# Kernel optimization log

Measured on AMD Instinct MI355X. Metric: run time of the kernel, lower is better.

## Reference

```python
import jax, jax.numpy as jnp
import numpy as np

BASE_RES = 0.2
RES_FACTOR = (1.0 - BASE_RES) * 0.9
N_ATOMS = 1024
LATENT = 128
WINDOW = 512
HOP = WINDOW // 2
RES_SAMPLES = 32768
N_FRAMES = RES_SAMPLES // HOP  # 128


def setup_inputs() -> dict:
    key = jax.random.key(0)
    ks = jax.random.split(key, 6)
    x = jax.random.normal(ks[0], (16, 64, LATENT), dtype=jnp.float32)
    W_sel = jax.random.normal(ks[1], (N_ATOMS, LATENT), dtype=jnp.float32) * 0.1
    b_sel = jnp.zeros((N_ATOMS,), dtype=jnp.float32)
    W_mom = jax.random.normal(ks[2], (N_FRAMES, LATENT), dtype=jnp.float32) * 0.1
    b_mom = jnp.zeros((N_FRAMES,), dtype=jnp.float32)
    atoms = jax.random.normal(ks[3], (N_ATOMS, RES_SAMPLES), dtype=jnp.float32) * 0.01
    return {"x": x, "W_sel": W_sel, "b_sel": b_sel, "W_mom": W_mom, "b_mom": b_mom, "atoms": atoms}


def _hann_periodic(n):
    # torch.hann_window default (periodic=True)
    return 0.5 * (1.0 - jnp.cos(2.0 * jnp.pi * jnp.arange(n) / n))


def reference(x, W_sel, b_sel, W_mom, b_mom, atoms):
    # momentum: sigmoid -> affine -> log-cumsum-exp decay per frame
    mom = BASE_RES + jax.nn.sigmoid(jnp.einsum('bel,fl->bef', x, W_mom) + b_mom) * RES_FACTOR
    mom = jnp.exp(jnp.cumsum(jnp.log(1e-12 + mom), axis=-1))  # (B,E,F)

    # softmax atom selection and mixing
    sel = jax.nn.softmax(jnp.einsum('bel,al->bea', x, W_sel) + b_sel, axis=-1)
    res = jnp.einsum('bea,as->bes', sel, atoms)  # (B,E,S)

    # windowed_audio: pad by hop, unfold, apply hann window
    padded = jnp.pad(res, ((0, 0), (0, 0), (0, HOP)))
    idx = jnp.arange(N_FRAMES)[:, None] * HOP + jnp.arange(WINDOW)[None, :]
    frames = padded[..., idx] * _hann_periodic(WINDOW)  # (B,E,F,W)

    # per-frame unit norm, then momentum scaling
    norm = jnp.linalg.norm(frames, axis=-1, keepdims=True)
    frames = frames / (norm + 1e-8)
    frames = frames * mom[..., None]

    # overlap-add with hop = WINDOW//2 (no extra window)
    B, E = frames.shape[0], frames.shape[1]
    first = frames[..., :HOP].reshape(B, E, -1)
    second = frames[..., HOP:].reshape(B, E, -1)
    out = jnp.pad(first, ((0, 0), (0, 0), (0, HOP))) + jnp.pad(second, ((0, 0), (0, 0), (HOP, 0)))
    return out[..., :RES_SAMPLES], mom
```

## Files before the change

kernel.cpp:

```cpp
#include <hip/hip_runtime.h>


typedef __attribute__((ext_vector_type(8))) short short8;
typedef __attribute__((ext_vector_type(4))) float f32x4;

typedef __attribute__((address_space(1))) void GV;
typedef __attribute__((address_space(3))) void LV;

__device__ __forceinline__ unsigned short f2bf(float f) {
    union { float f; unsigned u; } c; c.f = f;
    unsigned u = c.u;
    u = (u + 0x7FFFu + ((u >> 16) & 1u)) >> 16;
    return (unsigned short)u;
}
__device__ __forceinline__ float bf2f(unsigned short h) {
    union { unsigned u; float f; } c; c.u = ((unsigned)h) << 16; return c.f;
}

__global__ __launch_bounds__(256) void k_convert(
        const float* __restrict__ x, const float* __restrict__ Wsel,
        unsigned short* __restrict__ xbf, unsigned short* __restrict__ wbf) {
    const int i = (blockIdx.x * 256 + threadIdx.x) * 4;
    {
        float4 v = *(const float4*)(x + i);
        uint2 q;
        q.x = (unsigned)f2bf(v.x) | ((unsigned)f2bf(v.y) << 16);
        q.y = (unsigned)f2bf(v.z) | ((unsigned)f2bf(v.w) << 16);
        *(uint2*)(xbf + i) = q;
    }
    {
        float4 v = *(const float4*)(Wsel + i);
        uint2 q;
        q.x = (unsigned)f2bf(v.x) | ((unsigned)f2bf(v.y) << 16);
        q.y = (unsigned)f2bf(v.z) | ((unsigned)f2bf(v.w) << 16);
        *(uint2*)(wbf + i) = q;
    }
}

__global__ __launch_bounds__(256) void k_head_gemm(
        const unsigned short* __restrict__ A, const unsigned short* __restrict__ Bm,
        float* __restrict__ logits) {
    __shared__ __align__(16) unsigned short lA[128 * 32];
    __shared__ __align__(16) unsigned short lB[128 * 32];
    const int tid = threadIdx.x;
    const int wave = tid >> 6;
    const int lane = tid & 63;
    const int l15 = lane & 15, quad = lane >> 4;
    const int i0 = blockIdx.x * 128;
    const int j0 = blockIdx.y * 128;
    const int wi = wave >> 1, wj = wave & 1;
    const int rsel = lane >> 2;
    const int koff = (lane & 3) * 8;

    f32x4 acc[4][4] = {};

    for (int kt = 0; kt < 4; ++kt) {
        const int kbase = kt * 32;
#pragma unroll
        for (int c = 0; c < 2; ++c) {
            const int row = c * 64 + wave * 16 + rsel;
            const unsigned short* ga = A + (size_t)(i0 + row) * 128 + kbase + koff;
            const unsigned short* gb = Bm + (size_t)(j0 + row) * 128 + kbase + koff;
            unsigned short* la = lA + (c * 64 + wave * 16) * 32;
            unsigned short* lb = lB + (c * 64 + wave * 16) * 32;
            __builtin_amdgcn_global_load_lds((GV*)ga, (LV*)la, 16, 0, 0);
            __builtin_amdgcn_global_load_lds((GV*)gb, (LV*)lb, 16, 0, 0);
        }
        __syncthreads();

        short8 af[4], bf[4];
#pragma unroll
        for (int ti = 0; ti < 4; ++ti)
            af[ti] = *(const short8*)(lA + (wi * 64 + ti * 16 + l15) * 32 + quad * 8);
#pragma unroll
        for (int tj = 0; tj < 4; ++tj)
            bf[tj] = *(const short8*)(lB + (wj * 64 + tj * 16 + l15) * 32 + quad * 8);
#pragma unroll
        for (int ti = 0; ti < 4; ++ti)
#pragma unroll
            for (int tj = 0; tj < 4; ++tj)
                acc[ti][tj] = __builtin_amdgcn_mfma_f32_16x16x32_bf16(
                    af[ti], bf[tj], acc[ti][tj], 0, 0, 0);
        __syncthreads();
    }

#pragma unroll
    for (int ti = 0; ti < 4; ++ti) {
#pragma unroll
        for (int tj = 0; tj < 4; ++tj) {
            const int mrow = j0 + wj * 64 + tj * 16 + l15;
            const int abase = i0 + wi * 64 + ti * 16 + quad * 4;
            f32x4 v = acc[ti][tj];
            float4 o; o.x = v[0]; o.y = v[1]; o.z = v[2]; o.w = v[3];
            *(float4*)(logits + (size_t)mrow * 1024 + abase) = o;
        }
    }
}

__global__ __launch_bounds__(256) void k_softmax_mom(
        const float* __restrict__ logits_g, const float* __restrict__ bsel,
        const float* __restrict__ x, const float* __restrict__ Wmom,
        const float* __restrict__ bmom, unsigned short* __restrict__ sel,
        float* __restrict__ momout) {
    __shared__ float xs[128];
    __shared__ float logits[1024];
    __shared__ float mvals[128];
    __shared__ float wred[4];
    __shared__ float sstat[2];
    const int tid = threadIdx.x;
    const int m = blockIdx.x;

    if (tid < 32) *(float4*)&xs[tid * 4] = *(const float4*)(x + (size_t)m * 128 + tid * 4);
    for (int a = tid; a < 1024; a += 256)
        logits[a] = logits_g[(size_t)m * 1024 + a] + bsel[a];
    __syncthreads();

    if (tid < 128) {
        const float4* w = (const float4*)(Wmom + (size_t)tid * 128);
        float acc = 0.f;
#pragma unroll
        for (int k = 0; k < 32; ++k) {
            float4 wv = w[k]; float4 xv = *(const float4*)&xs[k * 4];
            acc += wv.x * xv.x + wv.y * xv.y + wv.z * xv.z + wv.w * xv.w;
        }
        acc += bmom[tid];
        float sig = 1.f / (1.f + __expf(-acc));
        mvals[tid] = 0.2f + sig * 0.72f;
    }
    __syncthreads();

    float mx = -1e30f;
    for (int a = tid; a < 1024; a += 256) mx = fmaxf(mx, logits[a]);
#pragma unroll
    for (int off = 32; off; off >>= 1) mx = fmaxf(mx, __shfl_xor(mx, off, 64));
    if ((tid & 63) == 0) wred[tid >> 6] = mx;
    __syncthreads();
    if (tid == 0) sstat[0] = fmaxf(fmaxf(wred[0], wred[1]), fmaxf(wred[2], wred[3]));
    __syncthreads();
    mx = sstat[0];

    float psum = 0.f;
    for (int a = tid; a < 1024; a += 256) {
        float e = __expf(logits[a] - mx);
        logits[a] = e;
        psum += e;
    }
#pragma unroll
    for (int off = 32; off; off >>= 1) psum += __shfl_xor(psum, off, 64);
    if ((tid & 63) == 0) wred[tid >> 6] = psum;
    __syncthreads();
    if (tid == 0) sstat[1] = wred[0] + wred[1] + wred[2] + wred[3];
    __syncthreads();
    const float inv = 1.f / sstat[1];
    for (int a = tid; a < 1024; a += 256)
        sel[(size_t)m * 1024 + a] = f2bf(logits[a] * inv);

    if (tid == 0) {
        float p = 1.f;
        for (int f = 0; f < 128; ++f) {
            p *= (mvals[f] + 1e-12f);
            momout[(size_t)m * 128 + f] = p;
        }
    }
}

__global__ __launch_bounds__(256) void k_transpose(
        const float* __restrict__ atoms, unsigned short* __restrict__ atomsT) {
    __shared__ float t[64][65];
    const int tid = threadIdx.x;
    const int s0 = blockIdx.x * 64;
    const int a0 = blockIdx.y * 64;

    {
        const int r0 = tid >> 4;
        const int c4 = (tid & 15) * 4;
        for (int rr = r0; rr < 64; rr += 16) {
            float4 v = *(const float4*)(atoms + (size_t)(a0 + rr) * 32768 + s0 + c4);
            t[rr][c4] = v.x; t[rr][c4 + 1] = v.y; t[rr][c4 + 2] = v.z; t[rr][c4 + 3] = v.w;
        }
    }
    __syncthreads();
    {
        const int sl = tid >> 2;
        const int seg = (tid & 3) * 16;
        unsigned short* dst = atomsT + (size_t)(s0 + sl) * 1024 + a0 + seg;
        unsigned pk[8];
#pragma unroll
        for (int i = 0; i < 16; i += 2) {
            unsigned short h0 = f2bf(t[seg + i][sl]);
            unsigned short h1 = f2bf(t[seg + i + 1][sl]);
            pk[i >> 1] = (unsigned)h0 | ((unsigned)h1 << 16);
        }
        uint4 q0; q0.x = pk[0]; q0.y = pk[1]; q0.z = pk[2]; q0.w = pk[3];
        uint4 q1; q1.x = pk[4]; q1.y = pk[5]; q1.z = pk[6]; q1.w = pk[7];
        *(uint4*)(dst) = q0;
        *(uint4*)(dst + 8) = q1;
    }
}

__global__ __launch_bounds__(256) void k_gemm(
        const unsigned short* __restrict__ A, const unsigned short* __restrict__ Bm,
        unsigned short* __restrict__ res) {
    __shared__ __align__(16) unsigned short lA[128 * 32];
    __shared__ __align__(16) unsigned short lB[128 * 32];
    const int tid = threadIdx.x;
    const int wave = tid >> 6;
    const int lane = tid & 63;
    const int l15 = lane & 15, quad = lane >> 4;
    const int bid = blockIdx.x;
    const int s_tile = ((bid >> 6) << 3) | (bid & 7);
    const int m_tile = (bid >> 3) & 7;
    const int j0 = m_tile * 128;
    const int i0 = s_tile * 128;
    const int wi = wave >> 1, wj = wave & 1;
    const int rsel = lane >> 2;
    const int koff = (lane & 3) * 8;

    f32x4 acc[4][4] = {};

    for (int kt = 0; kt < 32; ++kt) {
        const int kbase = kt * 32;
#pragma unroll
        for (int c = 0; c < 2; ++c) {
            const int row = c * 64 + wave * 16 + rsel;
            const unsigned short* ga = A + (size_t)(i0 + row) * 1024 + kbase + koff;
            const unsigned short* gb = Bm + (size_t)(j0 + row) * 1024 + kbase + koff;
            unsigned short* la = lA + (c * 64 + wave * 16) * 32;
            unsigned short* lb = lB + (c * 64 + wave * 16) * 32;
            __builtin_amdgcn_global_load_lds((GV*)ga, (LV*)la, 16, 0, 0);
            __builtin_amdgcn_global_load_lds((GV*)gb, (LV*)lb, 16, 0, 0);
        }
        __syncthreads();

        short8 af[4], bf[4];
#pragma unroll
        for (int ti = 0; ti < 4; ++ti)
            af[ti] = *(const short8*)(lA + (wi * 64 + ti * 16 + l15) * 32 + quad * 8);
#pragma unroll
        for (int tj = 0; tj < 4; ++tj)
            bf[tj] = *(const short8*)(lB + (wj * 64 + tj * 16 + l15) * 32 + quad * 8);
#pragma unroll
        for (int ti = 0; ti < 4; ++ti)
#pragma unroll
            for (int tj = 0; tj < 4; ++tj)
                acc[ti][tj] = __builtin_amdgcn_mfma_f32_16x16x32_bf16(
                    af[ti], bf[tj], acc[ti][tj], 0, 0, 0);
        __syncthreads();
    }

#pragma unroll
    for (int ti = 0; ti < 4; ++ti) {
#pragma unroll
        for (int tj = 0; tj < 4; ++tj) {
            const int mrow = j0 + wj * 64 + tj * 16 + l15;
            const int sbase = i0 + wi * 64 + ti * 16 + quad * 4;
            f32x4 v = acc[ti][tj];
            uint2 q;
            q.x = (unsigned)f2bf(v[0]) | ((unsigned)f2bf(v[1]) << 16);
            q.y = (unsigned)f2bf(v[2]) | ((unsigned)f2bf(v[3]) << 16);
            *(uint2*)(res + (size_t)mrow * 32768 + sbase) = q;
        }
    }
}

__global__ __launch_bounds__(256) void k_final(
        const unsigned short* __restrict__ res, const float* __restrict__ mom,
        float* __restrict__ out) {
    __shared__ __align__(16) unsigned short row[32768];
    __shared__ float hann[512];
    __shared__ float scale[128];
    const int tid = threadIdx.x;
    const int m = blockIdx.x;

#pragma unroll
    for (int j = 0; j < 16; ++j)
        *(uint4*)(row + j * 2048 + tid * 8) =
            *(const uint4*)(res + (size_t)m * 32768 + j * 2048 + tid * 8);
    for (int i = tid; i < 512; i += 256)
        hann[i] = 0.5f * (1.f - cosf(6.283185307179586f * (float)i / 512.f));
    __syncthreads();

    const int wave = tid >> 6, lane = tid & 63;
    for (int f = wave; f < 128; f += 4) {
        float s = 0.f;
#pragma unroll
        for (int jj = 0; jj < 4; ++jj) {
            const int i = jj * 128 + lane * 2;
            const int idx = f * 256 + i;
            float v0 = 0.f, v1 = 0.f;
            if (idx < 32768) {
                unsigned pr = *(const unsigned*)&row[idx];
                v0 = bf2f((unsigned short)pr);
                v1 = bf2f((unsigned short)(pr >> 16));
            }
            float w0 = v0 * hann[i], w1 = v1 * hann[i + 1];
            s += w0 * w0 + w1 * w1;
        }
#pragma unroll
        for (int off = 32; off; off >>= 1) s += __shfl_xor(s, off, 64);
        if (lane == 0) scale[f] = mom[(size_t)m * 128 + f] / (sqrtf(s) + 1e-8f);
    }
    __syncthreads();

#pragma unroll 4
    for (int j = 0; j < 32; ++j) {
        const int s0 = j * 1024 + tid * 4;
        const int f1 = s0 >> 8, i1 = s0 & 255;
        const float sc1 = scale[f1];
        const float sc0 = f1 ? scale[f1 - 1] : 0.f;
        uint2 rp = *(const uint2*)&row[s0];
        float4 o;
        o.x = bf2f((unsigned short)rp.x)         * (hann[i1]     * sc1 + hann[i1 + 256] * sc0);
        o.y = bf2f((unsigned short)(rp.x >> 16)) * (hann[i1 + 1] * sc1 + hann[i1 + 257] * sc0);
        o.z = bf2f((unsigned short)rp.y)         * (hann[i1 + 2] * sc1 + hann[i1 + 258] * sc0);
        o.w = bf2f((unsigned short)(rp.y >> 16)) * (hann[i1 + 3] * sc1 + hann[i1 + 259] * sc0);
        *(float4*)(out + (size_t)m * 32768 + s0) = o;
    }
}

extern "C" void kernel_launch(void* const* d_in, const int* in_sizes, int n_in,
                              void* d_out, int out_size, void* d_ws, size_t ws_size,
                              hipStream_t stream) {
    const float* x     = (const float*)d_in[0];
    const float* Wsel  = (const float*)d_in[1];
    const float* bsel  = (const float*)d_in[2];
    const float* Wmom  = (const float*)d_in[3];
    const float* bmom  = (const float*)d_in[4];
    const float* atoms = (const float*)d_in[5];

    float* out    = (float*)d_out;
    float* momout = out + (size_t)1024 * 32768;

    unsigned char* ws = (unsigned char*)d_ws;
    unsigned short* atomsT = (unsigned short*)(ws);
    unsigned short* sel    = (unsigned short*)(ws + 67108864);
    unsigned short* res    = (unsigned short*)(ws + 69206016);
    float*          logits = (float*)res;
    unsigned short* xbf    = (unsigned short*)(ws + 69206016 + 4194304);
    unsigned short* wbf    = (unsigned short*)(ws + 69206016 + 4194304 + 262144);

    k_convert<<<128, 256, 0, stream>>>(x, Wsel, xbf, wbf);
    k_head_gemm<<<dim3(8, 8), 256, 0, stream>>>(wbf, xbf, logits);
    k_softmax_mom<<<1024, 256, 0, stream>>>(logits, bsel, x, Wmom, bmom, sel, momout);
    k_transpose<<<dim3(512, 16), 256, 0, stream>>>(atoms, atomsT);
    k_gemm<<<2048, 256, 0, stream>>>(atomsT, sel, res);
    k_final<<<1024, 256, 0, stream>>>(res, momout, out);
}
```

Before: 413.0 us.

## Stage GEMM epilogue through LDS, stream k_final from global, transpose Wmom

The big GEMM now writes its bf16 tile into padded shared memory first, then stores full rows with coalesced 16-byte writes instead of scattered 8-byte stores. k_final drops its 64KB shared-memory row copy and reads res straight from global, computing half-frame norm partials per 256-sample chunk, which lowers LDS use and raises occupancy. The momentum projection reads a transposed Wmom (built in k_convert) so that its loads are coalesced, and one barrier is removed. The risks are extra LDS traffic in the GEMM epilogue and res being read twice from global/L2 in k_final.

New measurement: 402.9 us. 2.4% less time.

```diff
diff --git a/kernel.cpp b/kernel.cpp
--- a/kernel.cpp
+++ b/kernel.cpp
@@ -19,7 +19,9 @@
 
 __global__ __launch_bounds__(256) void k_convert(
         const float* __restrict__ x, const float* __restrict__ Wsel,
-        unsigned short* __restrict__ xbf, unsigned short* __restrict__ wbf) {
+        const float* __restrict__ Wmom,
+        unsigned short* __restrict__ xbf, unsigned short* __restrict__ wbf,
+        float* __restrict__ WmomT) {
     const int i = (blockIdx.x * 256 + threadIdx.x) * 4;
     {
         float4 v = *(const float4*)(x + i);
@@ -34,6 +36,16 @@
         q.x = (unsigned)f2bf(v.x) | ((unsigned)f2bf(v.y) << 16);
         q.y = (unsigned)f2bf(v.z) | ((unsigned)f2bf(v.w) << 16);
         *(uint2*)(wbf + i) = q;
+    }
+    if (blockIdx.x < 8) {
+        const int f  = blockIdx.x * 16 + (threadIdx.x >> 4);
+        const int kc = (threadIdx.x & 15) * 8;
+        float4 a = *(const float4*)(Wmom + (size_t)f * 128 + kc);
+        float4 b = *(const float4*)(Wmom + (size_t)f * 128 + kc + 4);
+        WmomT[(kc + 0) * 128 + f] = a.x; WmomT[(kc + 1) * 128 + f] = a.y;
+        WmomT[(kc + 2) * 128 + f] = a.z; WmomT[(kc + 3) * 128 + f] = a.w;
+        WmomT[(kc + 4) * 128 + f] = b.x; WmomT[(kc + 5) * 128 + f] = b.y;
+        WmomT[(kc + 6) * 128 + f] = b.z; WmomT[(kc + 7) * 128 + f] = b.w;
     }
 }
 
@@ -99,7 +111,7 @@
 
 __global__ __launch_bounds__(256) void k_softmax_mom(
         const float* __restrict__ logits_g, const float* __restrict__ bsel,
-        const float* __restrict__ x, const float* __restrict__ Wmom,
+        const float* __restrict__ x, const float* __restrict__ WmomT,
         const float* __restrict__ bmom, unsigned short* __restrict__ sel,
         float* __restrict__ momout) {
     __shared__ float xs[128];
@@ -116,18 +128,13 @@
     __syncthreads();
 
     if (tid < 128) {
-        const float4* w = (const float4*)(Wmom + (size_t)tid * 128);
-        float acc = 0.f;
-#pragma unroll
-        for (int k = 0; k < 32; ++k) {
-            float4 wv = w[k]; float4 xv = *(const float4*)&xs[k * 4];
-            acc += wv.x * xv.x + wv.y * xv.y + wv.z * xv.z + wv.w * xv.w;
-        }
-        acc += bmom[tid];
+        float acc = bmom[tid];
+#pragma unroll 8
+        for (int k = 0; k < 128; ++k)
+            acc += xs[k] * WmomT[k * 128 + tid];
         float sig = 1.f / (1.f + __expf(-acc));
         mvals[tid] = 0.2f + sig * 0.72f;
     }
-    __syncthreads();
 
     float mx = -1e30f;
     for (int a = tid; a < 1024; a += 256) mx = fmaxf(mx, logits[a]);
@@ -201,8 +208,9 @@
 __global__ __launch_bounds__(256) void k_gemm(
         const unsigned short* __restrict__ A, const unsigned short* __restrict__ Bm,
         unsigned short* __restrict__ res) {
-    __shared__ __align__(16) unsigned short lA[128 * 32];
-    __shared__ __align__(16) unsigned short lB[128 * 32];
+    __shared__ __align__(16) unsigned short buf[17408];
+    unsigned short* lA = buf;
+    unsigned short* lB = buf + 4096;
     const int tid = threadIdx.x;
     const int wave = tid >> 6;
     const int lane = tid & 63;
@@ -252,53 +260,73 @@
     for (int ti = 0; ti < 4; ++ti) {
 #pragma unroll
         for (int tj = 0; tj < 4; ++tj) {
-            const int mrow = j0 + wj * 64 + tj * 16 + l15;
-            const int sbase = i0 + wi * 64 + ti * 16 + quad * 4;
+            const int mloc = wj * 64 + tj * 16 + l15;
+            const int sloc = wi * 64 + ti * 16 + quad * 4;
             f32x4 v = acc[ti][tj];
             uint2 q;
             q.x = (unsigned)f2bf(v[0]) | ((unsigned)f2bf(v[1]) << 16);
             q.y = (unsigned)f2bf(v[2]) | ((unsigned)f2bf(v[3]) << 16);
-            *(uint2*)(res + (size_t)mrow * 32768 + sbase) = q;
-        }
+            *(uint2*)(buf + mloc * 136 + sloc) = q;
+        }
+    }
+    __syncthreads();
+    {
+        const int r = tid >> 1;
+        const int h = tid & 1;
+        unsigned short* grow = res + (size_t)(j0 + r) * 32768 + i0 + h * 64;
+        const unsigned short* lrow = buf + r * 136 + h * 64;
+#pragma unroll
+        for (int j = 0; j < 8; ++j)
+            *(uint4*)(grow + j * 8) = *(const uint4*)(lrow + j * 8);
     }
 }
 
 __global__ __launch_bounds__(256) void k_final(
         const unsigned short* __restrict__ res, const float* __restrict__ mom,
         float* __restrict__ out) {
-    __shared__ __align__(16) unsigned short row[32768];
     __shared__ float hann[512];
-    __shared__ float scale[128];
+    __shared__ float P0[128];
+    __shared__ float P1[128];
+    __shared__ float scl[129];
     const int tid = threadIdx.x;
     const int m = blockIdx.x;
-
-#pragma unroll
-    for (int j = 0; j < 16; ++j)
-        *(uint4*)(row + j * 2048 + tid * 8) =
-            *(const uint4*)(res + (size_t)m * 32768 + j * 2048 + tid * 8);
-    for (int i = tid; i < 512; i += 256)
-        hann[i] = 0.5f * (1.f - cosf(6.283185307179586f * (float)i / 512.f));
+    const unsigned short* row = res + (size_t)m * 32768;
+
+    hann[tid]       = 0.5f * (1.f - cosf(6.283185307179586f * (float)tid / 512.f));
+    hann[tid + 256] = 0.5f * (1.f - cosf(6.283185307179586f * (float)(tid + 256) / 512.f));
+    if (tid == 0) scl[0] = 0.f;
     __syncthreads();
 
     const int wave = tid >> 6, lane = tid & 63;
-    for (int f = wave; f < 128; f += 4) {
-        float s = 0.f;
-#pragma unroll
-        for (int jj = 0; jj < 4; ++jj) {
-            const int i = jj * 128 + lane * 2;
-            const int idx = f * 256 + i;
-            float v0 = 0.f, v1 = 0.f;
-            if (idx < 32768) {
-                unsigned pr = *(const unsigned*)&row[idx];
-                v0 = bf2f((unsigned short)pr);
-                v1 = bf2f((unsigned short)(pr >> 16));
-            }
-            float w0 = v0 * hann[i], w1 = v1 * hann[i + 1];
-            s += w0 * w0 + w1 * w1;
-        }
-#pragma unroll
-        for (int off = 32; off; off >>= 1) s += __shfl_xor(s, off, 64);
-        if (lane == 0) scale[f] = mom[(size_t)m * 128 + f] / (sqrtf(s) + 1e-8f);
+    const int ih = (lane & 31) * 8;
+    for (int cp = wave; cp < 64; cp += 4) {
+        const unsigned short* p = row + cp * 512 + lane * 8;
+        uint4 q = *(const uint4*)p;
+        float s0 = 0.f, s1 = 0.f;
+        const unsigned w[4] = {q.x, q.y, q.z, q.w};
+#pragma unroll
+        for (int j = 0; j < 4; ++j) {
+            float v0 = bf2f((unsigned short)w[j]);
+            float v1 = bf2f((unsigned short)(w[j] >> 16));
+            float a0 = v0 * hann[ih + j * 2],       a1 = v1 * hann[ih + j * 2 + 1];
+            float b0 = v0 * hann[256 + ih + j * 2], b1 = v1 * hann[256 + ih + j * 2 + 1];
+            s0 += a0 * a0 + a1 * a1;
+            s1 += b0 * b0 + b1 * b1;
+        }
+#pragma unroll
+        for (int off = 1; off <= 16; off <<= 1) {
+            s0 += __shfl_xor(s0, off, 64);
+            s1 += __shfl_xor(s1, off, 64);
+        }
+        if ((lane & 31) == 0) {
+            const int c = 2 * cp + (lane >> 5);
+            P0[c] = s0; P1[c] = s1;
+        }
+    }
+    __syncthreads();
+    if (tid < 128) {
+        const float n2 = P0[tid] + ((tid < 127) ? P1[tid + 1] : 0.f);
+        scl[tid + 1] = mom[(size_t)m * 128 + tid] / (sqrtf(n2) + 1e-8f);
     }
     __syncthreads();
 
@@ -306,9 +334,9 @@
     for (int j = 0; j < 32; ++j) {
         const int s0 = j * 1024 + tid * 4;
         const int f1 = s0 >> 8, i1 = s0 & 255;
-        const float sc1 = scale[f1];
-        const float sc0 = f1 ? scale[f1 - 1] : 0.f;
-        uint2 rp = *(const uint2*)&row[s0];
+        const float sc1 = scl[f1 + 1];
+        const float sc0 = scl[f1];
+        uint2 rp = *(const uint2*)(row + s0);
         float4 o;
         o.x = bf2f((unsigned short)rp.x)         * (hann[i1]     * sc1 + hann[i1 + 256] * sc0);
         o.y = bf2f((unsigned short)(rp.x >> 16)) * (hann[i1 + 1] * sc1 + hann[i1 + 257] * sc0);
@@ -338,10 +366,11 @@
     float*          logits = (float*)res;
     unsigned short* xbf    = (unsigned short*)(ws + 69206016 + 4194304);
     unsigned short* wbf    = (unsigned short*)(ws + 69206016 + 4194304 + 262144);
-
-    k_convert<<<128, 256, 0, stream>>>(x, Wsel, xbf, wbf);
+    float*          WmomT  = (float*)(ws + 69206016 + 4194304 + 524288);
+
+    k_convert<<<128, 256, 0, stream>>>(x, Wsel, Wmom, xbf, wbf, WmomT);
     k_head_gemm<<<dim3(8, 8), 256, 0, stream>>>(wbf, xbf, logits);
-    k_softmax_mom<<<1024, 256, 0, stream>>>(logits, bsel, x, Wmom, bmom, sel, momout);
+    k_softmax_mom<<<1024, 256, 0, stream>>>(logits, bsel, x, WmomT, bmom, sel, momout);
     k_transpose<<<dim3(512, 16), 256, 0, stream>>>(atoms, atomsT);
     k_gemm<<<2048, 256, 0, stream>>>(atomsT, sel, res);
     k_final<<<1024, 256, 0, stream>>>(res, momout, out);
```
